# Optimization experiments

Hardware: AMD Instinct MI355X
Metric: run time of the kernel (lower is better)

## Reference

```python
import jax, jax.numpy as jnp
import numpy as np

T, N = 64, 1048576  # bitstream length, number of parallel unary channels


def setup_inputs() -> dict:
    key = jax.random.key(0)
    kbits = jax.random.fold_in(key, 1)
    # unary bitstream: each bit is 0 or 1 (Bernoulli(0.5)); stored as float,
    # matching bstype=torch.float output / int8-on-{0,1} internal math exactly.
    bits = (jax.random.uniform(kbits, (T, N)) < 0.5).astype(jnp.float32)
    trace0 = jnp.zeros((N,), jnp.float32)  # JKFF state, torch inits zeros(1)
    return {"input": bits, "trace0": trace0}


def reference(input, trace0):
    # UnarySqrt with emit=False, mode='unipolar', jk_trace=True.
    # Per torch forward (python precedence: `1 - trace & input` == (1-trace)&input):
    #   output = ((1 - trace) & input) + trace
    #   trace' = JKFF(J=output, K=1)  ->  Q' = J & ~Q = output & (1 - trace)
    # On {0,1} bits, AND == multiply; the add is disjoint so stays exact.
    def step(trace, x):
        out = (1.0 - trace) * x + trace
        trace_next = out * (1.0 - trace)
        return trace_next, out

    _, outs = jax.lax.scan(step, trace0, input)  # outs: [T, N]
    return outs
```

## Files before the change

### kernel.cpp

```cpp
#include <hip/hip_runtime.h>


typedef float v4f __attribute__((ext_vector_type(4)));

__global__ __launch_bounds__(256) void UnarySqrt_kernel(
    const v4f* __restrict__ in,
    const v4f* __restrict__ trace0,
    v4f* __restrict__ out,
    int stride)
{
    int idx = blockIdx.x * blockDim.x + threadIdx.x;
    if (idx >= stride) return;

    v4f tr = trace0[idx];

    v4f buf[8];
    #pragma unroll
    for (int j = 0; j < 8; ++j) {
        buf[j] = in[(size_t)j * (size_t)stride + (size_t)idx];
    }

    #pragma unroll
    for (int t = 0; t < 64; ++t) {
        v4f x = buf[t & 7];
        if (t + 8 < 64) {
            buf[t & 7] = in[(size_t)(t + 8) * (size_t)stride + (size_t)idx];
        }
        v4f p = x * (1.0f - tr);
        v4f o = tr + p;
        __builtin_nontemporal_store(o, &out[(size_t)t * (size_t)stride + (size_t)idx]);
        tr = p;
    }
}

extern "C" void kernel_launch(void* const* d_in, const int* in_sizes, int n_in,
                              void* d_out, int out_size, void* d_ws, size_t ws_size,
                              hipStream_t stream) {
    const float* bits   = (const float*)d_in[0];
    const float* trace0 = (const float*)d_in[1];

    int N = in_sizes[1];
    int stride = N / 4;

    int block = 256;
    int grid = (stride + block - 1) / block;

    UnarySqrt_kernel<<<grid, block, 0, stream>>>(
        (const v4f*)bits,
        (const v4f*)trace0,
        (v4f*)d_out,
        stride);
}
```

Baseline: 468.4 us.

## Parallelize time recurrence via chunked affine scan across warps

Splits the 64-step scan into 8 chunks of 8 steps, each handled by a separate wavefront. Each chunk computes its end state for both possible starting traces (0 and 1), shares the pair through LDS, and combines prefixes as an affine map before replaying its chunk to produce outputs. This exposes more parallelism per column and shortens each thread's serial dependency chain. In exchange it adds some compute, an LDS exchange and a barrier, and uses fewer columns per block. A generic fallback kernel covers other shapes.

Result: faster. 449.0 us (-4.2%).

```diff
diff --git a/kernel.cpp b/kernel.cpp
--- a/kernel.cpp
+++ b/kernel.cpp
@@ -1,34 +1,72 @@
 #include <hip/hip_runtime.h>
+#include <stdint.h>
 
 
 typedef float v4f __attribute__((ext_vector_type(4)));
 
-__global__ __launch_bounds__(256) void UnarySqrt_kernel(
+#define CHUNKS 8
+#define CSTEPS 8
+
+__global__ __launch_bounds__(512) void UnarySqrt_kernel(
     const v4f* __restrict__ in,
     const v4f* __restrict__ trace0,
     v4f* __restrict__ out,
     int stride)
 {
+    __shared__ v4f lds0[CHUNKS][64];
+    __shared__ v4f lds1[CHUNKS][64];
+
+    const int tid   = threadIdx.x;
+    const int lane  = tid & 63;
+    const int chunk = tid >> 6;
+    const size_t g  = (size_t)blockIdx.x * 64 + lane;
+
+    v4f buf[CSTEPS];
+    #pragma unroll
+    for (int j = 0; j < CSTEPS; ++j) {
+        buf[j] = in[(size_t)(chunk * CSTEPS + j) * (size_t)stride + g];
+    }
+
+    v4f tr0 = {0.f, 0.f, 0.f, 0.f};
+    v4f tr1 = {1.f, 1.f, 1.f, 1.f};
+    #pragma unroll
+    for (int j = 0; j < CSTEPS; ++j) {
+        tr0 = buf[j] * (1.0f - tr0);
+        tr1 = buf[j] * (1.0f - tr1);
+    }
+    lds0[chunk][lane] = tr0;
+    lds1[chunk][lane] = tr1;
+    __syncthreads();
+
+    v4f s = trace0[g];
+    for (int k = 0; k < chunk; ++k) {
+        v4f a = lds0[k][lane];
+        v4f b = lds1[k][lane];
+        s = a + s * (b - a);
+    }
+
+    v4f tr = s;
+    #pragma unroll
+    for (int j = 0; j < CSTEPS; ++j) {
+        v4f p = buf[j] * (1.0f - tr);
+        v4f o = tr + p;
+        __builtin_nontemporal_store(
+            o, &out[(size_t)(chunk * CSTEPS + j) * (size_t)stride + g]);
+        tr = p;
+    }
+}
+
+__global__ __launch_bounds__(256) void UnarySqrt_generic(
+    const v4f* __restrict__ in, const v4f* __restrict__ trace0,
+    v4f* __restrict__ out, int stride, int T)
+{
     int idx = blockIdx.x * blockDim.x + threadIdx.x;
     if (idx >= stride) return;
-
     v4f tr = trace0[idx];
-
-    v4f buf[8];
-    #pragma unroll
-    for (int j = 0; j < 8; ++j) {
-        buf[j] = in[(size_t)j * (size_t)stride + (size_t)idx];
-    }
-
-    #pragma unroll
-    for (int t = 0; t < 64; ++t) {
-        v4f x = buf[t & 7];
-        if (t + 8 < 64) {
-            buf[t & 7] = in[(size_t)(t + 8) * (size_t)stride + (size_t)idx];
-        }
+    for (int t = 0; t < T; ++t) {
+        v4f x = in[(size_t)t * stride + idx];
         v4f p = x * (1.0f - tr);
-        v4f o = tr + p;
-        __builtin_nontemporal_store(o, &out[(size_t)t * (size_t)stride + (size_t)idx]);
+        out[(size_t)t * stride + idx] = tr + p;
         tr = p;
     }
 }
@@ -40,14 +78,17 @@
     const float* trace0 = (const float*)d_in[1];
 
     int N = in_sizes[1];
+    int T = in_sizes[0] / N;
     int stride = N / 4;
 
-    int block = 256;
-    int grid = (stride + block - 1) / block;
-
-    UnarySqrt_kernel<<<grid, block, 0, stream>>>(
-        (const v4f*)bits,
-        (const v4f*)trace0,
-        (v4f*)d_out,
-        stride);
+    if (T == 64 && (N % 256) == 0) {
+        int grid = stride / 64;
+        UnarySqrt_kernel<<<grid, 512, 0, stream>>>(
+            (const v4f*)bits, (const v4f*)trace0, (v4f*)d_out, stride);
+    } else {
+        int block = 256;
+        int grid = (stride + block - 1) / block;
+        UnarySqrt_generic<<<grid, block, 0, stream>>>(
+            (const v4f*)bits, (const v4f*)trace0, (v4f*)d_out, stride, T);
+    }
 }
```

## Stage input chunks through LDS via global_load_lds and use normal stores

Applied to the files above, without the earlier changes.

Replaces the register ring-buffer prefetch with chunked asynchronous global-to-LDS loads (16 rows per chunk, 4 chunks), waiting on vmcnt before consuming each chunk from shared memory. Output stores are no longer nontemporal. A generic fallback kernel handles shapes other than T=64 and N divisible by 1024. The chunk loop waits for all loads before computing, so there is no overlap between loading the next chunk and computing the current one, and the 64KB LDS per block may limit occupancy.

Measured after the change: 484.5 us. +3.4%, slower.

```diff
diff --git a/kernel.cpp b/kernel.cpp
--- a/kernel.cpp
+++ b/kernel.cpp
@@ -1,34 +1,70 @@
 #include <hip/hip_runtime.h>
+#include <stdint.h>
 
 
 typedef float v4f __attribute__((ext_vector_type(4)));
 
+#define AS1 __attribute__((address_space(1)))
+#define AS3 __attribute__((address_space(3)))
+
+#define CHUNK_ROWS 16
+#define NCHUNKS 4
+
 __global__ __launch_bounds__(256) void UnarySqrt_kernel(
-    const v4f* __restrict__ in,
-    const v4f* __restrict__ trace0,
-    v4f* __restrict__ out,
-    int stride)
+    const float* __restrict__ in,
+    const float* __restrict__ trace0,
+    float* __restrict__ out,
+    int stride4)
+{
+    __shared__ v4f lds[CHUNK_ROWS * 256];
+
+    const int tid = threadIdx.x;
+    const size_t g = (size_t)blockIdx.x * 256 + tid;
+
+    const v4f* in4  = (const v4f*)in;
+    v4f*       out4 = (v4f*)out;
+
+    v4f tr = ((const v4f*)trace0)[g];
+
+    for (int c = 0; c < NCHUNKS; ++c) {
+        if (c > 0) {
+            asm volatile("s_waitcnt lgkmcnt(0)" ::: "memory");
+        }
+
+        #pragma unroll
+        for (int j = 0; j < CHUNK_ROWS; ++j) {
+            const v4f* gp = &in4[(size_t)(c * CHUNK_ROWS + j) * (size_t)stride4 + g];
+            v4f* lp = &lds[j * 256 + tid];
+            __builtin_amdgcn_global_load_lds(
+                (const AS1 void*)(const void*)gp,
+                (AS3 void*)(void*)lp,
+                16, 0, 0);
+        }
+
+        asm volatile("s_waitcnt vmcnt(0)" ::: "memory");
+
+        #pragma unroll
+        for (int j = 0; j < CHUNK_ROWS; ++j) {
+            v4f x = lds[j * 256 + tid];
+            v4f p = x * (1.0f - tr);
+            v4f o = tr + p;
+            out4[(size_t)(c * CHUNK_ROWS + j) * (size_t)stride4 + g] = o;
+            tr = p;
+        }
+    }
+}
+
+__global__ __launch_bounds__(256) void UnarySqrt_generic(
+    const v4f* __restrict__ in, const v4f* __restrict__ trace0,
+    v4f* __restrict__ out, int stride, int T)
 {
     int idx = blockIdx.x * blockDim.x + threadIdx.x;
     if (idx >= stride) return;
-
     v4f tr = trace0[idx];
-
-    v4f buf[8];
-    #pragma unroll
-    for (int j = 0; j < 8; ++j) {
-        buf[j] = in[(size_t)j * (size_t)stride + (size_t)idx];
-    }
-
-    #pragma unroll
-    for (int t = 0; t < 64; ++t) {
-        v4f x = buf[t & 7];
-        if (t + 8 < 64) {
-            buf[t & 7] = in[(size_t)(t + 8) * (size_t)stride + (size_t)idx];
-        }
+    for (int t = 0; t < T; ++t) {
+        v4f x = in[(size_t)t * stride + idx];
         v4f p = x * (1.0f - tr);
-        v4f o = tr + p;
-        __builtin_nontemporal_store(o, &out[(size_t)t * (size_t)stride + (size_t)idx]);
+        out[(size_t)t * stride + idx] = tr + p;
         tr = p;
     }
 }
@@ -40,14 +76,16 @@
     const float* trace0 = (const float*)d_in[1];
 
     int N = in_sizes[1];
-    int stride = N / 4;
+    int T = in_sizes[0] / N;
+    int stride4 = N / 4;
 
-    int block = 256;
-    int grid = (stride + block - 1) / block;
-
-    UnarySqrt_kernel<<<grid, block, 0, stream>>>(
-        (const v4f*)bits,
-        (const v4f*)trace0,
-        (v4f*)d_out,
-        stride);
+    if (T == 64 && (N % 1024) == 0) {
+        int grid = stride4 / 256;
+        UnarySqrt_kernel<<<grid, 256, 0, stream>>>(bits, trace0, (float*)d_out, stride4);
+    } else {
+        int block = 256;
+        int grid = (stride4 + block - 1) / block;
+        UnarySqrt_generic<<<grid, block, 0, stream>>>(
+            (const v4f*)bits, (const v4f*)trace0, (v4f*)d_out, stride4, T);
+    }
 }
```
